# Kernel tuning notes

Hardware: AMD Instinct MI355X
Metric: run time of the kernel (lower is better)

## Reference

```python
import jax, jax.numpy as jnp
import numpy as np

ROUTINGS = 3
EPS = 1e-7  # K.epsilon()

B, IN_CAPS, IN_DIM = 32, 2048, 16
NUM_CAPS, DIM_CAPS = 32, 16


def setup_inputs() -> dict:
    key = jax.random.key(0)
    k1, k2 = jax.random.split(key)
    x = jax.random.normal(k1, (B, IN_CAPS, IN_DIM), dtype=jnp.float32)
    # glorot-uniform-ish scale for capsule weights
    limit = np.sqrt(6.0 / (IN_DIM + DIM_CAPS)).astype(np.float32)
    W = jax.random.uniform(k2, (1, IN_CAPS, NUM_CAPS, DIM_CAPS, IN_DIM),
                           dtype=jnp.float32, minval=-limit, maxval=limit)
    return {"x": x, "W": W}


def _squash(v, axis=-1):
    s = jnp.sum(v * v, axis=axis, keepdims=True)
    scale = s / (1.0 + s) / jnp.sqrt(s + EPS)
    return scale * v


def reference(x, W):
    # inputs_hat[b,i,n,d] = sum_k W[0,i,n,d,k] * x[b,i,k]
    u = jnp.einsum('indk,bik->bind', W[0], x)  # [B, in_caps, num_caps, dim_caps]
    b = jnp.zeros(u.shape[:3], dtype=u.dtype)  # routing logits [B, in_caps, num_caps]
    outputs = None
    for i in range(ROUTINGS):
        c = jax.nn.softmax(b, axis=2)               # over num_capsule
        weighted = u * c[..., None]                 # [B, in, num, dim]
        outputs = _squash(jnp.sum(weighted, axis=1))  # [B, num, dim]
        if i < ROUTINGS - 1:
            # faithful to source: b += sum_d inputs_hat * c (NOT agreement with outputs)
            b = b + jnp.sum(weighted, axis=-1)
    return outputs
```

## Files before the change

kernel.cpp:

```cpp
#include <hip/hip_runtime.h>
#include <cstdint>
#include <cstddef>

#define LOG2E 1.4426950408889634f

template<int CTRL>
__device__ __forceinline__ float dpp_addf(float v) {
  const int s = __builtin_amdgcn_update_dpp(
      0, __builtin_bit_cast(int, v), CTRL, 0xF, 0xF, true);
  return v + __builtin_bit_cast(float, s);
}
#define DPP_XOR1     0xB1
#define DPP_XOR2     0x4E
#define DPP_HALF_MIR 0x141
#define DPP_ROW_MIR  0x140

__device__ __forceinline__ float rlane(float v, int l) {
  return __builtin_bit_cast(float,
      __builtin_amdgcn_readlane(__builtin_bit_cast(int, v), l));
}

__device__ __forceinline__ void gld_lds16(const float* g, float* l) {
  __builtin_amdgcn_global_load_lds(
      (const __attribute__((address_space(1))) void*)g,
      (__attribute__((address_space(3))) void*)l, 16, 0, 0);
}

__device__ __forceinline__ int swz(int b) { return b ^ ((b >> 3) & 7); }

__device__ __forceinline__ void stage_half(const float* Wg, float* buf,
                                           int wv, int ln) {
  #pragma unroll
  for (int t = 0; t < 2; ++t) {
    const int seg = ((wv << 1) + t) << 8;
    const int j   = swz((seg >> 2) + ln);
    gld_lds16(Wg + ((j >> 1) << 4) + ((j & 1) << 2), buf + seg);
  }
}

__device__ __forceinline__ void stage_tile(const float* WtI, float* buf,
                                           int wv, int ln) {
  stage_half(WtI,     buf,        wv, ln);
  stage_half(WtI + 8, buf + 4096, wv, ln);
}

__device__ __forceinline__ void stage_x(const float* Xi, float* dst, int tid) {
  if (tid < 128) {
    gld_lds16(Xi + ((size_t)(tid >> 2) << 15) + ((tid & 3) << 2),
              dst + ((tid >> 6) << 8));
  }
}

__device__ __forceinline__ void lds_barrier() {
  asm volatile("s_waitcnt lgkmcnt(0)\n\ts_barrier" ::: "memory");
}

template<bool ATOMIC>
__global__ __launch_bounds__(512)
void caps_main(const float* __restrict__ X, const float* __restrict__ Wt,
               float* __restrict__ part) {
  __shared__ float sW[8192];
  __shared__ float sX[2][512];
  __shared__ float sWs[32 * 20];
  __shared__ float sC[32 * 36];
  __shared__ float sPad[2688];
  if ((int)blockIdx.x == -1) sPad[threadIdx.x] = 1.f;

  const int tid  = threadIdx.x;
  const int wv   = tid >> 6, ln = tid & 63;
  const int t256 = tid & 255;
  const int bh   = tid >> 8;
  const int i0   = blockIdx.x << 2;

  stage_tile(Wt + ((size_t)i0 << 13), sW, wv, ln);
  stage_x(X + ((size_t)i0 << 4), sX[0], tid);

  const int bB = tid >> 4;
  const int n1 = tid & 15;
  const int j0 = t256 << 2;
  const int nr = t256 >> 3;

  float acc0[16], acc1[16];
  #pragma unroll
  for (int b = 0; b < 16; ++b) { acc0[b] = 0.f; acc1[b] = 0.f; }

  #pragma clang loop unroll(disable)
  for (int ii = 0; ii < 4; ++ii) {
    const int p = ii & 1;
    __syncthreads();

    const float4 wa0 = *(const float4*)&sW[swz(j0 + 0) << 2];
    const float4 wa1 = *(const float4*)&sW[swz(j0 + 1) << 2];
    const float4 wb0 = *(const float4*)&sW[swz(j0 + 2) << 2];
    const float4 wb1 = *(const float4*)&sW[swz(j0 + 3) << 2];
    const float4 wa2 = *(const float4*)&sW[4096 + (swz(j0 + 0) << 2)];
    const float4 wa3 = *(const float4*)&sW[4096 + (swz(j0 + 1) << 2)];
    const float4 wb2 = *(const float4*)&sW[4096 + (swz(j0 + 2) << 2)];
    const float4 wb3 = *(const float4*)&sW[4096 + (swz(j0 + 3) << 2)];

    lds_barrier();

    if (ii < 3) {
      stage_x(X + ((size_t)(i0 + ii + 1) << 4), sX[p ^ 1], tid);
      stage_tile(Wt + ((size_t)(i0 + ii + 1) << 13), sW, wv, ln);
    }

    if (tid < 256) {
      float pr[16] = { wa0.x+wb0.x, wa0.y+wb0.y, wa0.z+wb0.z, wa0.w+wb0.w,
                       wa1.x+wb1.x, wa1.y+wb1.y, wa1.z+wb1.z, wa1.w+wb1.w,
                       wa2.x+wb2.x, wa2.y+wb2.y, wa2.z+wb2.z, wa2.w+wb2.w,
                       wa3.x+wb3.x, wa3.y+wb3.y, wa3.z+wb3.z, wa3.w+wb3.w };
      #pragma unroll
      for (int q = 0; q < 16; ++q) {
        float v = pr[q];
        v = dpp_addf<DPP_XOR1>(v);
        v = dpp_addf<DPP_XOR2>(v);
        v = dpp_addf<DPP_HALF_MIR>(v);
        pr[q] = v;
      }
      if ((tid & 7) < 4) {
        const int m = tid & 3;
        const float4 w =
            (m & 2) ? ((m & 1) ? make_float4(pr[12], pr[13], pr[14], pr[15])
                               : make_float4(pr[8],  pr[9],  pr[10], pr[11]))
                    : ((m & 1) ? make_float4(pr[4],  pr[5],  pr[6],  pr[7])
                               : make_float4(pr[0],  pr[1],  pr[2],  pr[3]));
        *(float4*)&sWs[(t256 >> 3) * 20 + (m << 2)] = w;
      }
    }
    lds_barrier();

    {
      const float* xr = &sX[p][bB << 4];
      const float4 x0 = *(const float4*)(xr + 0);
      const float4 x1 = *(const float4*)(xr + 4);
      const float4 x2 = *(const float4*)(xr + 8);
      const float4 x3 = *(const float4*)(xr + 12);
      float t1 = 0.f, t2 = 0.f;
      #pragma unroll
      for (int c4 = 0; c4 < 4; ++c4) {
        const float4 A1 = *(const float4*)&sWs[n1 * 20 + (c4 << 2)];
        const float4 A2 = *(const float4*)&sWs[(n1 + 16) * 20 + (c4 << 2)];
        const float4 xc = (c4 == 0) ? x0 : (c4 == 1) ? x1 : (c4 == 2) ? x2 : x3;
        t1 += A1.x * xc.x + A1.y * xc.y + A1.z * xc.z + A1.w * xc.w;
        t2 += A2.x * xc.x + A2.y * xc.y + A2.z * xc.z + A2.w * xc.w;
      }
      const float l1a = t1 * 0.03125f, l1b = t2 * 0.03125f;
      const float e1a = exp2f(l1a * LOG2E), e1b = exp2f(l1b * LOG2E);
      float s1 = e1a + e1b;
      s1 = dpp_addf<DPP_XOR1>(s1); s1 = dpp_addf<DPP_XOR2>(s1);
      s1 = dpp_addf<DPP_HALF_MIR>(s1); s1 = dpp_addf<DPP_ROW_MIR>(s1);
      const float rs1 = __builtin_amdgcn_rcpf(s1);
      const float l2a = l1a + e1a * rs1 * t1;
      const float l2b = l1b + e1b * rs1 * t2;
      const float e2a = exp2f(l2a * LOG2E), e2b = exp2f(l2b * LOG2E);
      float s2 = e2a + e2b;
      s2 = dpp_addf<DPP_XOR1>(s2); s2 = dpp_addf<DPP_XOR2>(s2);
      s2 = dpp_addf<DPP_HALF_MIR>(s2); s2 = dpp_addf<DPP_ROW_MIR>(s2);
      const float rs2 = __builtin_amdgcn_rcpf(s2);
      sC[n1 * 36 + bB]        = e2a * rs2;
      sC[(n1 + 16) * 36 + bB] = e2b * rs2;
    }
    lds_barrier();

    float c2s[16];
    {
      const int cb = nr * 36 + (bh << 4);
      *(float4*)&c2s[0]  = *(const float4*)&sC[cb + 0];
      *(float4*)&c2s[4]  = *(const float4*)&sC[cb + 4];
      *(float4*)&c2s[8]  = *(const float4*)&sC[cb + 8];
      *(float4*)&c2s[12] = *(const float4*)&sC[cb + 12];
    }
    const float4 xv = *(const float4*)
        &sX[p][(bh << 8) + ((ln >> 2) << 4) + ((ln & 3) << 2)];
    #pragma unroll
    for (int st = 0; st < 16; ++st) {
      __builtin_amdgcn_sched_barrier(0);
      const int lb = st << 2;
      const float s00 = rlane(xv.x, lb + 0), s01 = rlane(xv.y, lb + 0),
                  s02 = rlane(xv.z, lb + 0), s03 = rlane(xv.w, lb + 0);
      const float s10 = rlane(xv.x, lb + 1), s11 = rlane(xv.y, lb + 1),
                  s12 = rlane(xv.z, lb + 1), s13 = rlane(xv.w, lb + 1);
      const float s20 = rlane(xv.x, lb + 2), s21 = rlane(xv.y, lb + 2),
                  s22 = rlane(xv.z, lb + 2), s23 = rlane(xv.w, lb + 2);
      const float s30 = rlane(xv.x, lb + 3), s31 = rlane(xv.y, lb + 3),
                  s32 = rlane(xv.z, lb + 3), s33 = rlane(xv.w, lb + 3);
      float u0 = wa0.x*s00 + wa0.y*s01 + wa0.z*s02 + wa0.w*s03
               + wa1.x*s10 + wa1.y*s11 + wa1.z*s12 + wa1.w*s13
               + wa2.x*s20 + wa2.y*s21 + wa2.z*s22 + wa2.w*s23
               + wa3.x*s30 + wa3.y*s31 + wa3.z*s32 + wa3.w*s33;
      float u1 = wb0.x*s00 + wb0.y*s01 + wb0.z*s02 + wb0.w*s03
               + wb1.x*s10 + wb1.y*s11 + wb1.z*s12 + wb1.w*s13
               + wb2.x*s20 + wb2.y*s21 + wb2.z*s22 + wb2.w*s23
               + wb3.x*s30 + wb3.y*s31 + wb3.z*s32 + wb3.w*s33;
      acc0[st] += c2s[st] * u0;
      acc1[st] += c2s[st] * u1;
    }
  }

  if constexpr (ATOMIC) {
    #pragma unroll
    for (int j = 0; j < 16; ++j) {
      const int bgl = (bh << 4) + j;
      float* dst = part + ((size_t)bgl << 9) + (t256 << 1);
      atomicAdd(dst, acc0[j]);
      atomicAdd(dst + 1, acc1[j]);
    }
  } else {
    float* wp = part + ((size_t)blockIdx.x << 14) + (t256 << 1);
    #pragma unroll
    for (int j = 0; j < 16; ++j) {
      const int bgl = (bh << 4) + j;
      *(float2*)(wp + ((size_t)bgl << 9)) = make_float2(acc0[j], acc1[j]);
    }
  }
}

__global__ __launch_bounds__(512)
void caps_reduce(const float* __restrict__ part, float* __restrict__ out) {
  __shared__ float sred[32][64];
  const int tid = threadIdx.x;
  const int bid = blockIdx.x;
  const int b  = bid >> 3;
  const int rb = bid & 7;
  const int pg = tid >> 4;
  const int sl = tid & 15;
  const float* src = part + (((size_t)pg << 4) << 14)
                   + (b << 9) + (rb << 6) + (sl << 2);
  float4 a = make_float4(0.f, 0.f, 0.f, 0.f);
  #pragma unroll 4
  for (int p = 0; p < 16; ++p) {
    const float4 v = *(const float4*)(src + ((size_t)p << 14));
    a.x += v.x; a.y += v.y; a.z += v.z; a.w += v.w;
  }
  *(float4*)&sred[pg][sl << 2] = a;
  __syncthreads();
  if (tid < 64) {
    float s = 0.f;
    #pragma unroll
    for (int g = 0; g < 32; ++g) s += sred[g][tid];
    float sq = s * s;
    sq += __shfl_xor(sq, 1); sq += __shfl_xor(sq, 2);
    sq += __shfl_xor(sq, 4); sq += __shfl_xor(sq, 8);
    const float scale = sq / (1.0f + sq) / sqrtf(sq + 1e-7f);
    out[(b << 9) + (rb << 6) + tid] = scale * s;
  }
}

__global__ __launch_bounds__(256)
void caps_squash(const float* __restrict__ sums, float* __restrict__ out) {
  const int e = (blockIdx.x << 8) + threadIdx.x;
  const float s = sums[e];
  float sq = s * s;
  sq += __shfl_xor(sq, 1); sq += __shfl_xor(sq, 2);
  sq += __shfl_xor(sq, 4); sq += __shfl_xor(sq, 8);
  const float scale = sq / (1.0f + sq) / sqrtf(sq + 1e-7f);
  out[e] = scale * s;
}

extern "C" void kernel_launch(void* const* d_in, const int* in_sizes, int n_in,
                              void* d_out, int out_size, void* d_ws, size_t ws_size,
                              hipStream_t stream) {
  const float* X  = (const float*)d_in[0];
  const float* Wt = (const float*)d_in[1];
  float* out = (float*)d_out;
  float* wsf = (float*)d_ws;
  const size_t need = (size_t)512 * 16384 * sizeof(float);
  if (ws_size >= need) {
    caps_main<false><<<512, 512, 0, stream>>>(X, Wt, wsf);
    caps_reduce<<<256, 512, 0, stream>>>(wsf, out);
  } else {
    float* acc = (ws_size >= (size_t)16384 * sizeof(float)) ? wsf : out;
    hipMemsetAsync(acc, 0, 16384 * sizeof(float), stream);
    caps_main<true><<<512, 512, 0, stream>>>(X, Wt, acc);
    caps_squash<<<64, 256, 0, stream>>>(acc, out);
  }
}
```

Before: 47.28 us.

## Split weight reduction across all waves and precompute half of u before barrier

The partial-sum reduction of W pairs is now split between the low and high thread halves (each handles 8 of 16 values) instead of only tid<256 doing all 16. The x staging for the next tile is moved after the first barrier, and half of the u projections (8 of 16 steps) are computed before the sC barrier so that work overlaps with the softmax/routing phase. The aim is to balance work across waves and fill barrier wait time, at the cost of extra registers (us0/us1) and fewer sched_barriers.

Result: faster. 44.56 us (-5.8%).

```diff
diff --git a/kernel.cpp b/kernel.cpp
--- a/kernel.cpp
+++ b/kernel.cpp
@@ -98,37 +98,43 @@
     const float4 wb2 = *(const float4*)&sW[4096 + (swz(j0 + 2) << 2)];
     const float4 wb3 = *(const float4*)&sW[4096 + (swz(j0 + 3) << 2)];
 
-    lds_barrier();
-
-    if (ii < 3) {
-      stage_x(X + ((size_t)(i0 + ii + 1) << 4), sX[p ^ 1], tid);
-      stage_tile(Wt + ((size_t)(i0 + ii + 1) << 13), sW, wv, ln);
-    }
-
-    if (tid < 256) {
-      float pr[16] = { wa0.x+wb0.x, wa0.y+wb0.y, wa0.z+wb0.z, wa0.w+wb0.w,
-                       wa1.x+wb1.x, wa1.y+wb1.y, wa1.z+wb1.z, wa1.w+wb1.w,
-                       wa2.x+wb2.x, wa2.y+wb2.y, wa2.z+wb2.z, wa2.w+wb2.w,
-                       wa3.x+wb3.x, wa3.y+wb3.y, wa3.z+wb3.z, wa3.w+wb3.w };
+    const float4 xv = *(const float4*)
+        &sX[p][(bh << 8) + ((ln >> 2) << 4) + ((ln & 3) << 2)];
+
+    {
+      const bool hi = tid >= 256;
+      float pr[8];
+      if (!hi) {
+        pr[0]=wa0.x+wb0.x; pr[1]=wa0.y+wb0.y; pr[2]=wa0.z+wb0.z; pr[3]=wa0.w+wb0.w;
+        pr[4]=wa1.x+wb1.x; pr[5]=wa1.y+wb1.y; pr[6]=wa1.z+wb1.z; pr[7]=wa1.w+wb1.w;
+      } else {
+        pr[0]=wa2.x+wb2.x; pr[1]=wa2.y+wb2.y; pr[2]=wa2.z+wb2.z; pr[3]=wa2.w+wb2.w;
+        pr[4]=wa3.x+wb3.x; pr[5]=wa3.y+wb3.y; pr[6]=wa3.z+wb3.z; pr[7]=wa3.w+wb3.w;
+      }
       #pragma unroll
-      for (int q = 0; q < 16; ++q) {
+      for (int q = 0; q < 8; ++q) {
         float v = pr[q];
         v = dpp_addf<DPP_XOR1>(v);
         v = dpp_addf<DPP_XOR2>(v);
         v = dpp_addf<DPP_HALF_MIR>(v);
         pr[q] = v;
       }
-      if ((tid & 7) < 4) {
-        const int m = tid & 3;
-        const float4 w =
-            (m & 2) ? ((m & 1) ? make_float4(pr[12], pr[13], pr[14], pr[15])
-                               : make_float4(pr[8],  pr[9],  pr[10], pr[11]))
-                    : ((m & 1) ? make_float4(pr[4],  pr[5],  pr[6],  pr[7])
-                               : make_float4(pr[0],  pr[1],  pr[2],  pr[3]));
-        *(float4*)&sWs[(t256 >> 3) * 20 + (m << 2)] = w;
+      const int m7 = tid & 7;
+      const int mb = hi ? 2 : 0;
+      if (m7 == mb || m7 == mb + 1) {
+        const float4 w = (m7 == mb)
+            ? make_float4(pr[0], pr[1], pr[2], pr[3])
+            : make_float4(pr[4], pr[5], pr[6], pr[7]);
+        *(float4*)&sWs[(t256 >> 3) * 20 + (m7 << 2)] = w;
       }
     }
+
     lds_barrier();
+
+    if (ii < 3) {
+      stage_x(X + ((size_t)(i0 + ii + 1) << 4), sX[p ^ 1], tid);
+      stage_tile(Wt + ((size_t)(i0 + ii + 1) << 13), sW, wv, ln);
+    }
 
     {
       const float* xr = &sX[p][bB << 4];
@@ -161,6 +167,30 @@
       sC[n1 * 36 + bB]        = e2a * rs2;
       sC[(n1 + 16) * 36 + bB] = e2b * rs2;
     }
+
+    float us0[8], us1[8];
+    #pragma unroll
+    for (int st = 0; st < 8; ++st) {
+      if ((st & 3) == 0) __builtin_amdgcn_sched_barrier(0);
+      const int lb = st << 2;
+      const float s00 = rlane(xv.x, lb + 0), s01 = rlane(xv.y, lb + 0),
+                  s02 = rlane(xv.z, lb + 0), s03 = rlane(xv.w, lb + 0);
+      const float s10 = rlane(xv.x, lb + 1), s11 = rlane(xv.y, lb + 1),
+                  s12 = rlane(xv.z, lb + 1), s13 = rlane(xv.w, lb + 1);
+      const float s20 = rlane(xv.x, lb + 2), s21 = rlane(xv.y, lb + 2),
+                  s22 = rlane(xv.z, lb + 2), s23 = rlane(xv.w, lb + 2);
+      const float s30 = rlane(xv.x, lb + 3), s31 = rlane(xv.y, lb + 3),
+                  s32 = rlane(xv.z, lb + 3), s33 = rlane(xv.w, lb + 3);
+      us0[st] = wa0.x*s00 + wa0.y*s01 + wa0.z*s02 + wa0.w*s03
+              + wa1.x*s10 + wa1.y*s11 + wa1.z*s12 + wa1.w*s13
+              + wa2.x*s20 + wa2.y*s21 + wa2.z*s22 + wa2.w*s23
+              + wa3.x*s30 + wa3.y*s31 + wa3.z*s32 + wa3.w*s33;
+      us1[st] = wb0.x*s00 + wb0.y*s01 + wb0.z*s02 + wb0.w*s03
+              + wb1.x*s10 + wb1.y*s11 + wb1.z*s12 + wb1.w*s13
+              + wb2.x*s20 + wb2.y*s21 + wb2.z*s22 + wb2.w*s23
+              + wb3.x*s30 + wb3.y*s31 + wb3.z*s32 + wb3.w*s33;
+    }
+
     lds_barrier();
 
     float c2s[16];
@@ -171,11 +201,14 @@
       *(float4*)&c2s[8]  = *(const float4*)&sC[cb + 8];
       *(float4*)&c2s[12] = *(const float4*)&sC[cb + 12];
     }
-    const float4 xv = *(const float4*)
-        &sX[p][(bh << 8) + ((ln >> 2) << 4) + ((ln & 3) << 2)];
-    #pragma unroll
-    for (int st = 0; st < 16; ++st) {
-      __builtin_amdgcn_sched_barrier(0);
+    #pragma unroll
+    for (int st = 0; st < 8; ++st) {
+      acc0[st] += c2s[st] * us0[st];
+      acc1[st] += c2s[st] * us1[st];
+    }
+    #pragma unroll
+    for (int st = 8; st < 16; ++st) {
+      if ((st & 3) == 0) __builtin_amdgcn_sched_barrier(0);
       const int lb = st << 2;
       const float s00 = rlane(xv.x, lb + 0), s01 = rlane(xv.y, lb + 0),
                   s02 = rlane(xv.z, lb + 0), s03 = rlane(xv.w, lb + 0);
```

## Double block size to 1024 threads, one output column per thread

Applied to the files above, without the earlier changes.

Moves caps_main to 1024-thread blocks in which each thread owns one (num,dim) output column instead of two. This halves per-thread W registers and FMA work, and the W-sum reduction now spans 16 lanes with an extra DPP step. Both the x-tile load and the next-tile prefetch are moved ahead of the routing-logit phase. The LDS padding array that limited occupancy is removed and the sched_barrier is relaxed to every fourth step. The risk is more threads contending at each barrier, and half the threads sit idle during the logit/softmax phase.

Measured after the change: 49.88 us. 5.5% more time.

```diff
diff --git a/kernel.cpp b/kernel.cpp
--- a/kernel.cpp
+++ b/kernel.cpp
@@ -28,20 +28,17 @@
 
 __device__ __forceinline__ int swz(int b) { return b ^ ((b >> 3) & 7); }
 
-__device__ __forceinline__ void stage_half(const float* Wg, float* buf,
-                                           int wv, int ln) {
-  #pragma unroll
-  for (int t = 0; t < 2; ++t) {
-    const int seg = ((wv << 1) + t) << 8;
-    const int j   = swz((seg >> 2) + ln);
-    gld_lds16(Wg + ((j >> 1) << 4) + ((j & 1) << 2), buf + seg);
-  }
-}
-
-__device__ __forceinline__ void stage_tile(const float* WtI, float* buf,
-                                           int wv, int ln) {
-  stage_half(WtI,     buf,        wv, ln);
-  stage_half(WtI + 8, buf + 4096, wv, ln);
+__device__ __forceinline__ void stage_half16(const float* Wg, float* buf,
+                                             int wv, int ln) {
+  const int seg = wv << 8;
+  const int j   = swz((seg >> 2) + ln);
+  gld_lds16(Wg + ((j >> 1) << 4) + ((j & 1) << 2), buf + seg);
+}
+
+__device__ __forceinline__ void stage_tile16(const float* WtI, float* buf,
+                                             int wv, int ln) {
+  stage_half16(WtI,     buf,        wv, ln);
+  stage_half16(WtI + 8, buf + 4096, wv, ln);
 }
 
 __device__ __forceinline__ void stage_x(const float* Xi, float* dst, int tid) {
@@ -56,33 +53,31 @@
 }
 
 template<bool ATOMIC>
-__global__ __launch_bounds__(512)
+__global__ __launch_bounds__(1024, 2)
 void caps_main(const float* __restrict__ X, const float* __restrict__ Wt,
                float* __restrict__ part) {
   __shared__ float sW[8192];
   __shared__ float sX[2][512];
   __shared__ float sWs[32 * 20];
   __shared__ float sC[32 * 36];
-  __shared__ float sPad[2688];
-  if ((int)blockIdx.x == -1) sPad[threadIdx.x] = 1.f;
 
   const int tid  = threadIdx.x;
   const int wv   = tid >> 6, ln = tid & 63;
-  const int t256 = tid & 255;
-  const int bh   = tid >> 8;
+  const int r    = tid & 511;
+  const int bh   = tid >> 9;
   const int i0   = blockIdx.x << 2;
 
-  stage_tile(Wt + ((size_t)i0 << 13), sW, wv, ln);
+  stage_tile16(Wt + ((size_t)i0 << 13), sW, wv, ln);
   stage_x(X + ((size_t)i0 << 4), sX[0], tid);
 
   const int bB = tid >> 4;
   const int n1 = tid & 15;
-  const int j0 = t256 << 2;
-  const int nr = t256 >> 3;
-
-  float acc0[16], acc1[16];
+  const int j0 = r << 1;
+  const int nr = r >> 4;
+
+  float acc0[16];
   #pragma unroll
-  for (int b = 0; b < 16; ++b) { acc0[b] = 0.f; acc1[b] = 0.f; }
+  for (int b = 0; b < 16; ++b) acc0[b] = 0.f;
 
   #pragma clang loop unroll(disable)
   for (int ii = 0; ii < 4; ++ii) {
@@ -91,57 +86,56 @@
 
     const float4 wa0 = *(const float4*)&sW[swz(j0 + 0) << 2];
     const float4 wa1 = *(const float4*)&sW[swz(j0 + 1) << 2];
-    const float4 wb0 = *(const float4*)&sW[swz(j0 + 2) << 2];
-    const float4 wb1 = *(const float4*)&sW[swz(j0 + 3) << 2];
     const float4 wa2 = *(const float4*)&sW[4096 + (swz(j0 + 0) << 2)];
     const float4 wa3 = *(const float4*)&sW[4096 + (swz(j0 + 1) << 2)];
-    const float4 wb2 = *(const float4*)&sW[4096 + (swz(j0 + 2) << 2)];
-    const float4 wb3 = *(const float4*)&sW[4096 + (swz(j0 + 3) << 2)];
-
-    lds_barrier();
-
-    if (ii < 3) {
-      stage_x(X + ((size_t)(i0 + ii + 1) << 4), sX[p ^ 1], tid);
-      stage_tile(Wt + ((size_t)(i0 + ii + 1) << 13), sW, wv, ln);
-    }
-
-    if (tid < 256) {
-      float pr[16] = { wa0.x+wb0.x, wa0.y+wb0.y, wa0.z+wb0.z, wa0.w+wb0.w,
-                       wa1.x+wb1.x, wa1.y+wb1.y, wa1.z+wb1.z, wa1.w+wb1.w,
-                       wa2.x+wb2.x, wa2.y+wb2.y, wa2.z+wb2.z, wa2.w+wb2.w,
-                       wa3.x+wb3.x, wa3.y+wb3.y, wa3.z+wb3.z, wa3.w+wb3.w };
+
+    const float4 xv = *(const float4*)
+        &sX[p][(bh << 8) + ((ln >> 2) << 4) + ((ln & 3) << 2)];
+
+    {
+      const bool hi = tid >= 512;
+      float pr[8];
+      if (!hi) {
+        pr[0]=wa0.x; pr[1]=wa0.y; pr[2]=wa0.z; pr[3]=wa0.w;
+        pr[4]=wa1.x; pr[5]=wa1.y; pr[6]=wa1.z; pr[7]=wa1.w;
+      } else {
+        pr[0]=wa2.x; pr[1]=wa2.y; pr[2]=wa2.z; pr[3]=wa2.w;
+        pr[4]=wa3.x; pr[5]=wa3.y; pr[6]=wa3.z; pr[7]=wa3.w;
+      }
       #pragma unroll
-      for (int q = 0; q < 16; ++q) {
+      for (int q = 0; q < 8; ++q) {
         float v = pr[q];
         v = dpp_addf<DPP_XOR1>(v);
         v = dpp_addf<DPP_XOR2>(v);
         v = dpp_addf<DPP_HALF_MIR>(v);
+        v = dpp_addf<DPP_ROW_MIR>(v);
         pr[q] = v;
       }
-      if ((tid & 7) < 4) {
-        const int m = tid & 3;
-        const float4 w =
-            (m & 2) ? ((m & 1) ? make_float4(pr[12], pr[13], pr[14], pr[15])
-                               : make_float4(pr[8],  pr[9],  pr[10], pr[11]))
-                    : ((m & 1) ? make_float4(pr[4],  pr[5],  pr[6],  pr[7])
-                               : make_float4(pr[0],  pr[1],  pr[2],  pr[3]));
-        *(float4*)&sWs[(t256 >> 3) * 20 + (m << 2)] = w;
-      }
-    }
+      const int l16 = ln & 15;
+      if (l16 < 2) {
+        const int m = (hi ? 2 : 0) + l16;
+        const float4 w = (l16 == 0)
+            ? make_float4(pr[0], pr[1], pr[2], pr[3])
+            : make_float4(pr[4], pr[5], pr[6], pr[7]);
+        *(float4*)&sWs[nr * 20 + (m << 2)] = w;
+      }
+    }
+
     lds_barrier();
 
-    {
+    if (ii < 3) {
+      stage_x(X + ((size_t)(i0 + ii + 1) << 4), sX[p ^ 1], tid);
+      stage_tile16(Wt + ((size_t)(i0 + ii + 1) << 13), sW, wv, ln);
+    }
+
+    if (tid < 512) {
       const float* xr = &sX[p][bB << 4];
-      const float4 x0 = *(const float4*)(xr + 0);
-      const float4 x1 = *(const float4*)(xr + 4);
-      const float4 x2 = *(const float4*)(xr + 8);
-      const float4 x3 = *(const float4*)(xr + 12);
       float t1 = 0.f, t2 = 0.f;
       #pragma unroll
       for (int c4 = 0; c4 < 4; ++c4) {
         const float4 A1 = *(const float4*)&sWs[n1 * 20 + (c4 << 2)];
         const float4 A2 = *(const float4*)&sWs[(n1 + 16) * 20 + (c4 << 2)];
-        const float4 xc = (c4 == 0) ? x0 : (c4 == 1) ? x1 : (c4 == 2) ? x2 : x3;
+        const float4 xc = *(const float4*)(xr + (c4 << 2));
         t1 += A1.x * xc.x + A1.y * xc.y + A1.z * xc.z + A1.w * xc.w;
         t2 += A2.x * xc.x + A2.y * xc.y + A2.z * xc.z + A2.w * xc.w;
       }
@@ -161,6 +155,7 @@
       sC[n1 * 36 + bB]        = e2a * rs2;
       sC[(n1 + 16) * 36 + bB] = e2b * rs2;
     }
+
     lds_barrier();
 
     float c2s[16];
@@ -171,11 +166,9 @@
       *(float4*)&c2s[8]  = *(const float4*)&sC[cb + 8];
       *(float4*)&c2s[12] = *(const float4*)&sC[cb + 12];
     }
-    const float4 xv = *(const float4*)
-        &sX[p][(bh << 8) + ((ln >> 2) << 4) + ((ln & 3) << 2)];
     #pragma unroll
     for (int st = 0; st < 16; ++st) {
-      __builtin_amdgcn_sched_barrier(0);
+      if ((st & 3) == 0) __builtin_amdgcn_sched_barrier(0);
       const int lb = st << 2;
       const float s00 = rlane(xv.x, lb + 0), s01 = rlane(xv.y, lb + 0),
                   s02 = rlane(xv.z, lb + 0), s03 = rlane(xv.w, lb + 0);
@@ -189,12 +182,7 @@
                + wa1.x*s10 + wa1.y*s11 + wa1.z*s12 + wa1.w*s13
                + wa2.x*s20 + wa2.y*s21 + wa2.z*s22 + wa2.w*s23
                + wa3.x*s30 + wa3.y*s31 + wa3.z*s32 + wa3.w*s33;
-      float u1 = wb0.x*s00 + wb0.y*s01 + wb0.z*s02 + wb0.w*s03
-               + wb1.x*s10 + wb1.y*s11 + wb1.z*s12 + wb1.w*s13
-               + wb2.x*s20 + wb2.y*s21 + wb2.z*s22 + wb2.w*s23
-               + wb3.x*s30 + wb3.y*s31 + wb3.z*s32 + wb3.w*s33;
       acc0[st] += c2s[st] * u0;
-      acc1[st] += c2s[st] * u1;
     }
   }
 
@@ -202,20 +190,19 @@
     #pragma unroll
     for (int j = 0; j < 16; ++j) {
       const int bgl = (bh << 4) + j;
-      float* dst = part + ((size_t)bgl << 9) + (t256 << 1);
-      atomicAdd(dst, acc0[j]);
-      atomicAdd(dst + 1, acc1[j]);
+      atomicAdd(part + ((size_t)bgl << 9) + r, acc0[j]);
     }
   } else {
-    float* wp = part + ((size_t)blockIdx.x << 14) + (t256 << 1);
+    float* wp = part + ((size_t)blockIdx.x << 14) + r;
     #pragma unroll
     for (int j = 0; j < 16; ++j) {
       const int bgl = (bh << 4) + j;
-      *(float2*)(wp + ((size_t)bgl << 9)) = make_float2(acc0[j], acc1[j]);
-    }
-  }
-}
-
+      wp[(size_t)bgl << 9] = acc0[j];
+    }
+  }
+}
+
+template<int NP>
 __global__ __launch_bounds__(512)
 void caps_reduce(const float* __restrict__ part, float* __restrict__ out) {
   __shared__ float sred[32][64];
@@ -225,11 +212,11 @@
   const int rb = bid & 7;
   const int pg = tid >> 4;
   const int sl = tid & 15;
-  const float* src = part + (((size_t)pg << 4) << 14)
+  const float* src = part + (((size_t)pg * NP) << 14)
                    + (b << 9) + (rb << 6) + (sl << 2);
   float4 a = make_float4(0.f, 0.f, 0.f, 0.f);
   #pragma unroll 4
-  for (int p = 0; p < 16; ++p) {
+  for (int p = 0; p < NP; ++p) {
     const float4 v = *(const float4*)(src + ((size_t)p << 14));
     a.x += v.x; a.y += v.y; a.z += v.z; a.w += v.w;
   }
@@ -267,12 +254,12 @@
   float* wsf = (float*)d_ws;
   const size_t need = (size_t)512 * 16384 * sizeof(float);
   if (ws_size >= need) {
-    caps_main<false><<<512, 512, 0, stream>>>(X, Wt, wsf);
-    caps_reduce<<<256, 512, 0, stream>>>(wsf, out);
+    caps_main<false><<<512, 1024, 0, stream>>>(X, Wt, wsf);
+    caps_reduce<16><<<256, 512, 0, stream>>>(wsf, out);
   } else {
     float* acc = (ws_size >= (size_t)16384 * sizeof(float)) ? wsf : out;
     hipMemsetAsync(acc, 0, 16384 * sizeof(float), stream);
-    caps_main<true><<<512, 512, 0, stream>>>(X, Wt, acc);
+    caps_main<true><<<512, 1024, 0, stream>>>(X, Wt, acc);
     caps_squash<<<64, 256, 0, stream>>>(acc, out);
   }
 }
```
